# Performance work log

Hardware: AMD Instinct MI355X
Metric: run time of the kernel (lower is better)

The kernel has to match this reference:

```python
import jax, jax.numpy as jnp
import numpy as np

N_PTS = 524288
N_LEVELS = 16
F_PER = 2
T = 1 << 19            # log2_hashmap_size = 19
BASE_RES = 16
BOUND = 1.0
PLS = float(np.exp2(np.log2(2048.0 * BOUND / N_LEVELS) / (N_LEVELS - 1)))
RES = [int(np.floor(BASE_RES * PLS ** l)) for l in range(N_LEVELS)]
OFFS = np.array([[(i >> 2) & 1, (i >> 1) & 1, i & 1] for i in range(8)], dtype=np.int32)  # [8,3] cube corners


def hashgrid_encode(x, tables):
    # x: [N,3] in [0,1]; tables: [L, T, F]
    offs = jnp.asarray(OFFS)
    offs_b = offs.astype(bool)
    feats = []
    for l in range(N_LEVELS):
        res = RES[l]
        pos = x * (res - 1)
        p0 = jnp.floor(pos)
        frac = pos - p0                                     # [N,3]
        corners = jnp.clip(p0.astype(jnp.int32)[:, None, :] + offs[None], 0, res - 1)  # [N,8,3]
        w = jnp.prod(jnp.where(offs_b[None], frac[:, None, :], 1.0 - frac[:, None, :]), axis=-1)  # [N,8]
        if res ** 3 <= T:
            idx = corners[..., 0] + res * corners[..., 1] + res * res * corners[..., 2]
        else:
            c = corners.astype(jnp.uint32)
            idx = (c[..., 0] ^ (c[..., 1] * jnp.uint32(2654435761)) ^ (c[..., 2] * jnp.uint32(805459861))) & jnp.uint32(T - 1)
            idx = idx.astype(jnp.int32)
        feats.append(jnp.einsum('nkf,nk->nf', tables[l][idx], w))  # trilinear interp
    return jnp.concatenate(feats, axis=-1)  # [N, 32]


def sh_encode(d):
    # degree-4 spherical harmonics basis, torch-ngp coefficients -> [N,16]
    x, y, z = d[..., 0], d[..., 1], d[..., 2]
    xy, xz, yz = x * y, x * z, y * z
    x2, y2, z2 = x * x, y * y, z * z
    return jnp.stack([
        jnp.full_like(x, 0.28209479177387814),
        -0.48860251190291987 * y,
        0.48860251190291987 * z,
        -0.48860251190291987 * x,
        1.0925484305920792 * xy,
        -1.0925484305920792 * yz,
        0.94617469575755997 * z2 - 0.31539156525252005,
        -1.0925484305920792 * xz,
        0.54627421529603959 * (x2 - y2),
        0.59004358992664352 * y * (-3.0 * x2 + y2),
        2.8906114426405538 * xy * z,
        0.45704579946446572 * y * (1.0 - 5.0 * z2),
        0.3731763325901154 * z * (5.0 * z2 - 3.0),
        0.45704579946446572 * x * (1.0 - 5.0 * z2),
        1.4453057213202769 * z * (x2 - y2),
        0.59004358992664352 * x * (x2 - 3.0 * y2),
    ], axis=-1)


def l2_normalize(v):
    return v / jnp.maximum(jnp.linalg.norm(v, axis=-1, keepdims=True), 1e-8)


def density(xyz, tables, ws0, ws1):
    xn = jnp.clip((xyz + BOUND) / (2.0 * BOUND), 0.0, 1.0)
    h = jax.nn.relu(hashgrid_encode(xn, tables) @ ws0)  # [N,64]
    h = h @ ws1                                          # [N,16]
    return h[..., 0], h[..., 1:]                         # sigma [N], geo_feat [N,15]


def setup_inputs() -> dict:
    key = jax.random.key(0)
    ks = jax.random.split(key, 11)
    x = jax.random.uniform(ks[0], (N_PTS, 6), minval=-1.0, maxval=1.0, dtype=jnp.float32)
    tables = jax.random.uniform(ks[1], (N_LEVELS, T, F_PER), minval=-1e-4, maxval=1e-4, dtype=jnp.float32)

    def lin(k, din, dout):
        s = 1.0 / float(np.sqrt(din))
        return jax.random.uniform(k, (din, dout), minval=-s, maxval=s, dtype=jnp.float32)

    return dict(
        x=x, tables=tables,
        ws0=lin(ks[2], 32, 64), ws1=lin(ks[3], 64, 16),
        wc0=lin(ks[4], 31, 64), wc1=lin(ks[5], 64, 64), wc2=lin(ks[6], 64, 3),
        wn0=lin(ks[7], 15, 64), wn1=lin(ks[8], 64, 3),
        wm0=lin(ks[9], 15, 32), bm0=jnp.zeros((32,), jnp.float32),
        wm1=lin(ks[10], 32, 1), bm1=jnp.zeros((1,), jnp.float32),
    )


def reference(x, tables, ws0, ws1, wc0, wc1, wc2, wn0, wn1, wm0, bm0, wm1, bm1):
    xyz, d = x[:, :3], x[:, 3:]

    # sigma + analytic normal = l2_normalize(-grad_x sigma)  (compute_normal=True path)
    def f(p):
        s, g = density(p, tables, ws0, ws1)
        return s.sum(), (s, g)

    (_, (sigma, geo_feat)), grad_density = jax.value_and_grad(f, has_aux=True)(xyz)
    normal = l2_normalize(-grad_density)

    # predicted normal head (bias-free 15->64->3)
    pred_normal = l2_normalize(jax.nn.relu(geo_feat @ wn0) @ wn1)

    # color head: SH(dir) ++ geo_feat -> 31->64->64->3, sigmoid
    h = jnp.concatenate([sh_encode(d), geo_feat], axis=-1)
    rgb = jax.nn.sigmoid(jax.nn.relu(jax.nn.relu(h @ wc0) @ wc1) @ wc2)

    # mirror-mask head: 15->32 LeakyReLU ->1 sigmoid (with biases)
    m = jax.nn.leaky_relu(geo_feat @ wm0 + bm0, negative_slope=0.01)
    is_mirror = jax.nn.sigmoid(m @ wm1 + bm1)

    return sigma, geo_feat, normal, pred_normal, rgb, is_mirror
```

## Files before the change

kernel.cpp:

```cpp
#include <hip/hip_runtime.h>
#include <math.h>

#define N_POINTS 524288
#define NLV      16
#define TSZ      524288
#define TMASK    (TSZ - 1)
#define ASTART   5
#define NA       (NLV - ASTART)

static_assert(NA == 11, "NA mismatch");

struct Params { int res[NLV]; };


struct Gather {
    float2 t0, t1, t2, t3, t4, t5, t6, t7;
    float fx, fy, fz;
};
struct Enc2 { float e0, e1; };
struct EncA { float e0, e1, a0x, a0y, a0z, a1x, a1y, a1z; };
struct L3v  { float lx, ly, lz; };

template<bool HASHED>
__device__ __forceinline__ Gather lv_issue(const float2* __restrict__ lt, const int res,
                                           const float xn0, const float xn1, const float xn2)
{
#pragma clang fp contract(off)
    Gather g;
    const float rf = (float)(res - 1);
    const float px = xn0 * rf, py = xn1 * rf, pz = xn2 * rf;
    const float bx = floorf(px), by = floorf(py), bz = floorf(pz);
    g.fx = px - bx; g.fy = py - by; g.fz = pz - bz;
    const int r1 = res - 1;
    const int ix = (int)bx, iy = (int)by, iz = (int)bz;
    const int cx0 = min(max(ix, 0), r1),     cx1 = min(max(ix + 1, 0), r1);
    const int cy0 = min(max(iy, 0), r1),     cy1 = min(max(iy + 1, 0), r1);
    const int cz0 = min(max(iz, 0), r1),     cz1 = min(max(iz + 1, 0), r1);
    unsigned i000, i001, i010, i011, i100, i101, i110, i111;
    if constexpr (HASHED) {
        const unsigned hx0 = (unsigned)cx0, hx1 = (unsigned)cx1;
        const unsigned hy0 = (unsigned)cy0 * 2654435761u, hy1 = (unsigned)cy1 * 2654435761u;
        const unsigned hz0 = (unsigned)cz0 * 805459861u,  hz1 = (unsigned)cz1 * 805459861u;
        const unsigned e00 = hy0 ^ hz0, e01 = hy0 ^ hz1, e10 = hy1 ^ hz0, e11 = hy1 ^ hz1;
        i000 = (hx0 ^ e00) & TMASK; i001 = (hx0 ^ e01) & TMASK;
        i010 = (hx0 ^ e10) & TMASK; i011 = (hx0 ^ e11) & TMASK;
        i100 = (hx1 ^ e00) & TMASK; i101 = (hx1 ^ e01) & TMASK;
        i110 = (hx1 ^ e10) & TMASK; i111 = (hx1 ^ e11) & TMASK;
    } else {
        const int b00 = res * (cy0 + res * cz0), b01 = res * (cy0 + res * cz1);
        const int b10 = res * (cy1 + res * cz0), b11 = res * (cy1 + res * cz1);
        i000 = (unsigned)(cx0 + b00); i001 = (unsigned)(cx0 + b01);
        i010 = (unsigned)(cx0 + b10); i011 = (unsigned)(cx0 + b11);
        i100 = (unsigned)(cx1 + b00); i101 = (unsigned)(cx1 + b01);
        i110 = (unsigned)(cx1 + b10); i111 = (unsigned)(cx1 + b11);
    }
    g.t0 = lt[i000]; g.t1 = lt[i001]; g.t2 = lt[i010]; g.t3 = lt[i011];
    g.t4 = lt[i100]; g.t5 = lt[i101]; g.t6 = lt[i110]; g.t7 = lt[i111];
    return g;
}

__device__ __forceinline__ Enc2 lv_enc(const Gather g)
{
#pragma clang fp contract(off)
    const float gx0 = 1.0f - g.fx, gx1 = g.fx;
    const float gy0 = 1.0f - g.fy, gy1 = g.fy;
    const float gz0 = 1.0f - g.fz, gz1 = g.fz;
    const float pxy00 = gx0 * gy0, pxy01 = gx0 * gy1, pxy10 = gx1 * gy0, pxy11 = gx1 * gy1;
    const float w000 = pxy00 * gz0, w001 = pxy00 * gz1, w010 = pxy01 * gz0, w011 = pxy01 * gz1;
    const float w100 = pxy10 * gz0, w101 = pxy10 * gz1, w110 = pxy11 * gz0, w111 = pxy11 * gz1;
    float e0 = 0.0f, e1 = 0.0f;
    e0 = e0 + w000 * g.t0.x; e1 = e1 + w000 * g.t0.y;
    e0 = e0 + w001 * g.t1.x; e1 = e1 + w001 * g.t1.y;
    e0 = e0 + w010 * g.t2.x; e1 = e1 + w010 * g.t2.y;
    e0 = e0 + w011 * g.t3.x; e1 = e1 + w011 * g.t3.y;
    e0 = e0 + w100 * g.t4.x; e1 = e1 + w100 * g.t4.y;
    e0 = e0 + w101 * g.t5.x; e1 = e1 + w101 * g.t5.y;
    e0 = e0 + w110 * g.t6.x; e1 = e1 + w110 * g.t6.y;
    e0 = e0 + w111 * g.t7.x; e1 = e1 + w111 * g.t7.y;
    Enc2 r; r.e0 = e0; r.e1 = e1; return r;
}

__device__ __forceinline__ EncA lv_enc_a(const Gather g)
{
#pragma clang fp contract(off)
    const float gx0 = 1.0f - g.fx, gx1 = g.fx;
    const float gy0 = 1.0f - g.fy, gy1 = g.fy;
    const float gz0 = 1.0f - g.fz, gz1 = g.fz;
    const float pxy00 = gx0 * gy0, pxy01 = gx0 * gy1, pxy10 = gx1 * gy0, pxy11 = gx1 * gy1;
    const float w000 = pxy00 * gz0, w001 = pxy00 * gz1, w010 = pxy01 * gz0, w011 = pxy01 * gz1;
    const float w100 = pxy10 * gz0, w101 = pxy10 * gz1, w110 = pxy11 * gz0, w111 = pxy11 * gz1;
    float e0 = 0.0f, e1 = 0.0f;
    e0 = e0 + w000 * g.t0.x; e1 = e1 + w000 * g.t0.y;
    e0 = e0 + w001 * g.t1.x; e1 = e1 + w001 * g.t1.y;
    e0 = e0 + w010 * g.t2.x; e1 = e1 + w010 * g.t2.y;
    e0 = e0 + w011 * g.t3.x; e1 = e1 + w011 * g.t3.y;
    e0 = e0 + w100 * g.t4.x; e1 = e1 + w100 * g.t4.y;
    e0 = e0 + w101 * g.t5.x; e1 = e1 + w101 * g.t5.y;
    e0 = e0 + w110 * g.t6.x; e1 = e1 + w110 * g.t6.y;
    e0 = e0 + w111 * g.t7.x; e1 = e1 + w111 * g.t7.y;
    const float pyz00 = gy0 * gz0, pyz01 = gy0 * gz1, pyz10 = gy1 * gz0, pyz11 = gy1 * gz1;
    const float pxz00 = gx0 * gz0, pxz01 = gx0 * gz1, pxz10 = gx1 * gz0, pxz11 = gx1 * gz1;
    float a0x = 0.f, a0y = 0.f, a0z = 0.f, a1x = 0.f, a1y = 0.f, a1z = 0.f;
    a0x = fmaf(-pyz00, g.t0.x, a0x); a1x = fmaf(-pyz00, g.t0.y, a1x);
    a0y = fmaf(-pxz00, g.t0.x, a0y); a1y = fmaf(-pxz00, g.t0.y, a1y);
    a0z = fmaf(-pxy00, g.t0.x, a0z); a1z = fmaf(-pxy00, g.t0.y, a1z);
    a0x = fmaf(-pyz01, g.t1.x, a0x); a1x = fmaf(-pyz01, g.t1.y, a1x);
    a0y = fmaf(-pxz01, g.t1.x, a0y); a1y = fmaf(-pxz01, g.t1.y, a1y);
    a0z = fmaf( pxy00, g.t1.x, a0z); a1z = fmaf( pxy00, g.t1.y, a1z);
    a0x = fmaf(-pyz10, g.t2.x, a0x); a1x = fmaf(-pyz10, g.t2.y, a1x);
    a0y = fmaf( pxz00, g.t2.x, a0y); a1y = fmaf( pxz00, g.t2.y, a1y);
    a0z = fmaf(-pxy01, g.t2.x, a0z); a1z = fmaf(-pxy01, g.t2.y, a1z);
    a0x = fmaf(-pyz11, g.t3.x, a0x); a1x = fmaf(-pyz11, g.t3.y, a1x);
    a0y = fmaf( pxz01, g.t3.x, a0y); a1y = fmaf( pxz01, g.t3.y, a1y);
    a0z = fmaf( pxy01, g.t3.x, a0z); a1z = fmaf( pxy01, g.t3.y, a1z);
    a0x = fmaf( pyz00, g.t4.x, a0x); a1x = fmaf( pyz00, g.t4.y, a1x);
    a0y = fmaf(-pxz10, g.t4.x, a0y); a1y = fmaf(-pxz10, g.t4.y, a1y);
    a0z = fmaf(-pxy10, g.t4.x, a0z); a1z = fmaf(-pxy10, g.t4.y, a1z);
    a0x = fmaf( pyz01, g.t5.x, a0x); a1x = fmaf( pyz01, g.t5.y, a1x);
    a0y = fmaf(-pxz11, g.t5.x, a0y); a1y = fmaf(-pxz11, g.t5.y, a1y);
    a0z = fmaf( pxy10, g.t5.x, a0z); a1z = fmaf( pxy10, g.t5.y, a1z);
    a0x = fmaf( pyz10, g.t6.x, a0x); a1x = fmaf( pyz10, g.t6.y, a1x);
    a0y = fmaf( pxz10, g.t6.x, a0y); a1y = fmaf( pxz10, g.t6.y, a1y);
    a0z = fmaf(-pxy11, g.t6.x, a0z); a1z = fmaf(-pxy11, g.t6.y, a1z);
    a0x = fmaf( pyz11, g.t7.x, a0x); a1x = fmaf( pyz11, g.t7.y, a1x);
    a0y = fmaf( pxz11, g.t7.x, a0y); a1y = fmaf( pxz11, g.t7.y, a1y);
    a0z = fmaf( pxy11, g.t7.x, a0z); a1z = fmaf( pxy11, g.t7.y, a1z);
    EncA r;
    r.e0 = e0; r.e1 = e1;
    r.a0x = a0x; r.a0y = a0y; r.a0z = a0z;
    r.a1x = a1x; r.a1y = a1y; r.a1z = a1z;
    return r;
}

__device__ __forceinline__ L3v bwd_part(const Gather g, const float g0, const float g1)
{
    const float gx0 = 1.0f - g.fx, gx1 = g.fx;
    const float gy0 = 1.0f - g.fy, gy1 = g.fy;
    const float gz0 = 1.0f - g.fz, gz1 = g.fz;
    const float pyz00 = gy0 * gz0, pyz01 = gy0 * gz1, pyz10 = gy1 * gz0, pyz11 = gy1 * gz1;
    const float pxz00 = gx0 * gz0, pxz01 = gx0 * gz1, pxz10 = gx1 * gz0, pxz11 = gx1 * gz1;
    const float pxy00 = gx0 * gy0, pxy01 = gx0 * gy1, pxy10 = gx1 * gy0, pxy11 = gx1 * gy1;
    const float s000 = fmaf(g0, g.t0.x, g1 * g.t0.y);
    const float s001 = fmaf(g0, g.t1.x, g1 * g.t1.y);
    const float s010 = fmaf(g0, g.t2.x, g1 * g.t2.y);
    const float s011 = fmaf(g0, g.t3.x, g1 * g.t3.y);
    const float s100 = fmaf(g0, g.t4.x, g1 * g.t4.y);
    const float s101 = fmaf(g0, g.t5.x, g1 * g.t5.y);
    const float s110 = fmaf(g0, g.t6.x, g1 * g.t6.y);
    const float s111 = fmaf(g0, g.t7.x, g1 * g.t7.y);
    float lx = 0.f, ly = 0.f, lz = 0.f;
    lx = fmaf(-pyz00, s000, lx); ly = fmaf(-pxz00, s000, ly); lz = fmaf(-pxy00, s000, lz);
    lx = fmaf(-pyz01, s001, lx); ly = fmaf(-pxz01, s001, ly); lz = fmaf( pxy00, s001, lz);
    lx = fmaf(-pyz10, s010, lx); ly = fmaf( pxz00, s010, ly); lz = fmaf(-pxy01, s010, lz);
    lx = fmaf(-pyz11, s011, lx); ly = fmaf( pxz01, s011, ly); lz = fmaf( pxy01, s011, lz);
    lx = fmaf( pyz00, s100, lx); ly = fmaf(-pxz10, s100, ly); lz = fmaf(-pxy10, s100, lz);
    lx = fmaf( pyz01, s101, lx); ly = fmaf(-pxz11, s101, ly); lz = fmaf( pxy10, s101, lz);
    lx = fmaf( pyz10, s110, lx); ly = fmaf( pxz10, s110, ly); lz = fmaf(-pxy11, s110, lz);
    lx = fmaf( pyz11, s111, lx); ly = fmaf( pxz11, s111, ly); lz = fmaf( pxy11, s111, lz);
    L3v r; r.lx = lx; r.ly = ly; r.lz = lz; return r;
}

__device__ __forceinline__ void clampedxn(const float* __restrict__ x, const int n,
                                          float& xn0, float& xn1, float& xn2)
{
    const float x0 = x[(size_t)n * 6 + 0];
    const float x1 = x[(size_t)n * 6 + 1];
    const float x2 = x[(size_t)n * 6 + 2];
    xn0 = fminf(fmaxf((x0 + 1.0f) * 0.5f, 0.0f), 1.0f);
    xn1 = fminf(fmaxf((x1 + 1.0f) * 0.5f, 0.0f), 1.0f);
    xn2 = fminf(fmaxf((x2 + 1.0f) * 0.5f, 0.0f), 1.0f);
}

#define ST_E(L, R) { we[(size_t)(2*(L))*N + n] = R.e0; we[(size_t)(2*(L)+1)*N + n] = R.e1; }
#define ST_A(L, R) { const int i_ = (L) - ASTART;                         \
        wa[(size_t)(0*NA + i_)*N + n] = R.a0x;                            \
        wa[(size_t)(1*NA + i_)*N + n] = R.a0y;                            \
        wa[(size_t)(2*NA + i_)*N + n] = R.a0z;                            \
        wa[(size_t)(3*NA + i_)*N + n] = R.a1x;                            \
        wa[(size_t)(4*NA + i_)*N + n] = R.a1y;                            \
        wa[(size_t)(5*NA + i_)*N + n] = R.a1z; }
#define PAIR_NN(LA, LB) {                                                              \
        const Gather gA = lv_issue<false>(tb + (size_t)(LA)*TSZ, P.res[LA], xn0, xn1, xn2); \
        const Gather gB = lv_issue<false>(tb + (size_t)(LB)*TSZ, P.res[LB], xn0, xn1, xn2); \
        const Enc2 rA = lv_enc(gA); ST_E(LA, rA)                                       \
        const Enc2 rB = lv_enc(gB); ST_E(LB, rB) }
#define PAIR_NA(LA, LB) {                                                              \
        const Gather gA = lv_issue<false>(tb + (size_t)(LA)*TSZ, P.res[LA], xn0, xn1, xn2); \
        const Gather gB = lv_issue<false>(tb + (size_t)(LB)*TSZ, P.res[LB], xn0, xn1, xn2); \
        const Enc2 rA = lv_enc(gA); ST_E(LA, rA)                                       \
        const EncA rB = lv_enc_a(gB); ST_E(LB, rB) ST_A(LB, rB) }
#define PAIR_AA(LA, LB) {                                                              \
        const Gather gA = lv_issue<true>(tb + (size_t)(LA)*TSZ, P.res[LA], xn0, xn1, xn2);  \
        const Gather gB = lv_issue<true>(tb + (size_t)(LB)*TSZ, P.res[LB], xn0, xn1, xn2);  \
        const EncA rA = lv_enc_a(gA); ST_E(LA, rA) ST_A(LA, rA)                        \
        const EncA rB = lv_enc_a(gB); ST_E(LB, rB) ST_A(LB, rB) }

__global__ __launch_bounds__(256) __attribute__((amdgpu_waves_per_eu(6, 6)))
void k_gather_lo(const float* __restrict__ x, const float* __restrict__ tables,
                 float* __restrict__ ws, Params P)
{
    const int n = blockIdx.x * 256 + threadIdx.x;
    if (n >= N_POINTS) return;
    const size_t N = (size_t)N_POINTS;
    float xn0, xn1, xn2;
    clampedxn(x, n, xn0, xn1, xn2);
    const float2* __restrict__ tb = (const float2*)tables;
    float* __restrict__ we = ws;
    float* __restrict__ wa = ws + 32 * N;

    PAIR_NN(0, 1)
    PAIR_NN(2, 3)
    PAIR_NA(4, 5)
    PAIR_AA(6, 7)
}

__global__ __launch_bounds__(256) __attribute__((amdgpu_waves_per_eu(6, 6)))
void k_gather_hi(const float* __restrict__ x, const float* __restrict__ tables,
                 float* __restrict__ ws, Params P)
{
    const int n = blockIdx.x * 256 + threadIdx.x;
    if (n >= N_POINTS) return;
    const size_t N = (size_t)N_POINTS;
    float xn0, xn1, xn2;
    clampedxn(x, n, xn0, xn1, xn2);
    const float2* __restrict__ tb = (const float2*)tables;
    float* __restrict__ we = ws;
    float* __restrict__ wa = ws + 32 * N;

    PAIR_AA(8, 9)
    PAIR_AA(10, 11)
    PAIR_AA(12, 13)
    PAIR_AA(14, 15)
}

__global__ __launch_bounds__(256) __attribute__((amdgpu_waves_per_eu(5, 8)))
void k_density(const float* __restrict__ x, const float* __restrict__ tables,
               const float* __restrict__ w_s0, const float* __restrict__ w_s1,
               const float* __restrict__ ws, float* __restrict__ wgeo,
               float* __restrict__ out, Params P)
{
    const int n = blockIdx.x * 256 + threadIdx.x;
    if (n >= N_POINTS) return;
    const size_t N = (size_t)N_POINTS;
    float xn0, xn1, xn2;
    clampedxn(x, n, xn0, xn1, xn2);
    const float2* __restrict__ tb = (const float2*)tables;
    const float* __restrict__ we = ws;
    const float* __restrict__ wa = ws + 32 * N;

    float enc[32];
    #pragma unroll
    for (int j = 0; j < 32; ++j) enc[j] = we[(size_t)j * N + n];

    float hd[16];
    #pragma unroll
    for (int m = 0; m < 16; ++m) hd[m] = 0.0f;
    unsigned long long mask = 0ull;
    {
        #pragma clang fp contract(off)
        for (int k = 0; k < 64; ++k) {
            float a = 0.0f;
            #pragma unroll
            for (int j = 0; j < 32; ++j) {
                const float p = enc[j] * w_s0[j * 64 + k];
                a = a + p;
            }
            const float hr = fmaxf(a, 0.0f);
            #pragma unroll
            for (int m = 0; m < 16; ++m) hd[m] = fmaf(hr, w_s1[k * 16 + m], hd[m]);
            if (a > 0.0f) mask |= (1ull << k);
        }
    }
    const float sigma = hd[0];

    out[n] = sigma;
    #pragma unroll
    for (int j = 0; j < 15; ++j) {
        out[N + (size_t)n * 15 + j] = hd[1 + j];
        wgeo[(size_t)j * N + n] = hd[1 + j];
    }

    float genc[32];
    #pragma unroll
    for (int j = 0; j < 32; ++j) genc[j] = 0.0f;
    for (int k = 0; k < 64; ++k) {
        const float ghk = ((mask >> k) & 1ull) ? w_s1[k * 16] : 0.0f;
        #pragma unroll
        for (int j = 0; j < 32; ++j) genc[j] = fmaf(w_s0[j * 64 + k], ghk, genc[j]);
    }

    float gx = 0.0f, gy = 0.0f, gz = 0.0f;
    {
        const Gather gA = lv_issue<false>(tb + 0 * (size_t)TSZ, P.res[0], xn0, xn1, xn2);
        const Gather gB = lv_issue<false>(tb + 1 * (size_t)TSZ, P.res[1], xn0, xn1, xn2);
        {
            const L3v d = bwd_part(gA, genc[0], genc[1]);
            const float rf = (float)(P.res[0] - 1);
            gx = fmaf(d.lx, rf, gx); gy = fmaf(d.ly, rf, gy); gz = fmaf(d.lz, rf, gz);
        }
        {
            const L3v d = bwd_part(gB, genc[2], genc[3]);
            const float rf = (float)(P.res[1] - 1);
            gx = fmaf(d.lx, rf, gx); gy = fmaf(d.ly, rf, gy); gz = fmaf(d.lz, rf, gz);
        }
    }
    {
        const Gather gA = lv_issue<false>(tb + 2 * (size_t)TSZ, P.res[2], xn0, xn1, xn2);
        const Gather gB = lv_issue<false>(tb + 3 * (size_t)TSZ, P.res[3], xn0, xn1, xn2);
        {
            const L3v d = bwd_part(gA, genc[4], genc[5]);
            const float rf = (float)(P.res[2] - 1);
            gx = fmaf(d.lx, rf, gx); gy = fmaf(d.ly, rf, gy); gz = fmaf(d.lz, rf, gz);
        }
        {
            const L3v d = bwd_part(gB, genc[6], genc[7]);
            const float rf = (float)(P.res[3] - 1);
            gx = fmaf(d.lx, rf, gx); gy = fmaf(d.ly, rf, gy); gz = fmaf(d.lz, rf, gz);
        }
    }
    {
        const Gather gA = lv_issue<false>(tb + 4 * (size_t)TSZ, P.res[4], xn0, xn1, xn2);
        const L3v d = bwd_part(gA, genc[8], genc[9]);
        const float rf = (float)(P.res[4] - 1);
        gx = fmaf(d.lx, rf, gx); gy = fmaf(d.ly, rf, gy); gz = fmaf(d.lz, rf, gz);
    }

    #pragma unroll
    for (int l = ASTART; l < NLV; ++l) {
        const int i = l - ASTART;
        const float rf = (float)(P.res[l] - 1);
        const float g0 = genc[2 * l], g1 = genc[2 * l + 1];
        const float a0x = wa[(size_t)(0*NA + i)*N + n];
        const float a0y = wa[(size_t)(1*NA + i)*N + n];
        const float a0z = wa[(size_t)(2*NA + i)*N + n];
        const float a1x = wa[(size_t)(3*NA + i)*N + n];
        const float a1y = wa[(size_t)(4*NA + i)*N + n];
        const float a1z = wa[(size_t)(5*NA + i)*N + n];
        gx = fmaf(rf, fmaf(g0, a0x, g1 * a1x), gx);
        gy = fmaf(rf, fmaf(g0, a0y, g1 * a1y), gy);
        gz = fmaf(rf, fmaf(g0, a0z, g1 * a1z), gz);
    }
    gx *= 0.5f; gy *= 0.5f; gz *= 0.5f;

    const float gnorm = sqrtf(gx * gx + gy * gy + gz * gz);
    const float ginv = 1.0f / fmaxf(gnorm, 1e-8f);

    out[16 * N + (size_t)n * 3 + 0] = -gx * ginv;
    out[16 * N + (size_t)n * 3 + 1] = -gy * ginv;
    out[16 * N + (size_t)n * 3 + 2] = -gz * ginv;
}

__global__ __launch_bounds__(256) __attribute__((amdgpu_waves_per_eu(4, 4)))
void k_color(const float* __restrict__ x,
             const float* __restrict__ wc0, const float* __restrict__ wc1,
             const float* __restrict__ wc2,
             const float* __restrict__ wn0, const float* __restrict__ wn1,
             const float* __restrict__ wm0, const float* __restrict__ bm0,
             const float* __restrict__ wm1, const float* __restrict__ bm1,
             const float* __restrict__ wgeo, float* __restrict__ out)
{
    const int n = blockIdx.x * 256 + threadIdx.x;
    if (n >= N_POINTS) return;
    const size_t N = (size_t)N_POINTS;

    float geo[15];
    #pragma unroll
    for (int j = 0; j < 15; ++j) geo[j] = wgeo[(size_t)j * N + n];

    float pn0 = 0.0f, pn1 = 0.0f, pn2 = 0.0f;
    for (int k = 0; k < 64; ++k) {
        float a = 0.0f;
        #pragma unroll
        for (int j = 0; j < 15; ++j) a = fmaf(geo[j], wn0[j * 64 + k], a);
        a = fmaxf(a, 0.0f);
        pn0 = fmaf(a, wn1[k * 3 + 0], pn0);
        pn1 = fmaf(a, wn1[k * 3 + 1], pn1);
        pn2 = fmaf(a, wn1[k * 3 + 2], pn2);
    }
    const float pnorm = sqrtf(pn0 * pn0 + pn1 * pn1 + pn2 * pn2);
    const float pinv = 1.0f / fmaxf(pnorm, 1e-8f);
    out[19 * N + (size_t)n * 3 + 0] = pn0 * pinv;
    out[19 * N + (size_t)n * 3 + 1] = pn1 * pinv;
    out[19 * N + (size_t)n * 3 + 2] = pn2 * pinv;

    float macc = 0.0f;
    for (int k = 0; k < 32; ++k) {
        float a = bm0[k];
        #pragma unroll
        for (int j = 0; j < 15; ++j) a = fmaf(geo[j], wm0[j * 32 + k], a);
        a = (a >= 0.0f) ? a : 0.01f * a;
        macc = fmaf(a, wm1[k], macc);
    }
    macc += bm1[0];
    out[25 * N + n] = 1.0f / (1.0f + expf(-macc));

    const float dx = x[(size_t)n * 6 + 3];
    const float dy = x[(size_t)n * 6 + 4];
    const float dz = x[(size_t)n * 6 + 5];
    float sh[16];
    const float xy = dx * dy, xz = dx * dz, yz = dy * dz;
    const float x2s = dx * dx, y2s = dy * dy, z2s = dz * dz;
    sh[0]  = 0.28209479177387814f;
    sh[1]  = -0.48860251190291987f * dy;
    sh[2]  =  0.48860251190291987f * dz;
    sh[3]  = -0.48860251190291987f * dx;
    sh[4]  =  1.0925484305920792f * xy;
    sh[5]  = -1.0925484305920792f * yz;
    sh[6]  =  0.94617469575756f * z2s - 0.31539156525252005f;
    sh[7]  = -1.0925484305920792f * xz;
    sh[8]  =  0.5462742152960396f * (x2s - y2s);
    sh[9]  =  0.5900435899266435f * dy * (-3.0f * x2s + y2s);
    sh[10] =  2.890611442640554f * xy * dz;
    sh[11] =  0.4570457994644657f * dy * (1.0f - 5.0f * z2s);
    sh[12] =  0.3731763325901154f * dz * (5.0f * z2s - 3.0f);
    sh[13] =  0.4570457994644657f * dx * (1.0f - 5.0f * z2s);
    sh[14] =  1.445305721320277f * dz * (x2s - y2s);
    sh[15] =  0.5900435899266435f * dx * (x2s - 3.0f * y2s);

    float cacc[64];
    #pragma unroll
    for (int k = 0; k < 64; ++k) cacc[k] = 0.0f;
    for (int kc = 0; kc < 64; ++kc) {
        float a = 0.0f;
        #pragma unroll
        for (int j = 0; j < 16; ++j) a = fmaf(sh[j], wc0[j * 64 + kc], a);
        #pragma unroll
        for (int j = 0; j < 15; ++j) a = fmaf(geo[j], wc0[(16 + j) * 64 + kc], a);
        const float c1v = fmaxf(a, 0.0f);
        const float* __restrict__ wrow = wc1 + kc * 64;
        #pragma unroll
        for (int k2 = 0; k2 < 64; ++k2) cacc[k2] = fmaf(c1v, wrow[k2], cacc[k2]);
    }
    float r0 = 0.0f, r1 = 0.0f, r2 = 0.0f;
    #pragma unroll
    for (int k = 0; k < 64; ++k) {
        const float a = fmaxf(cacc[k], 0.0f);
        r0 = fmaf(a, wc2[k * 3 + 0], r0);
        r1 = fmaf(a, wc2[k * 3 + 1], r1);
        r2 = fmaf(a, wc2[k * 3 + 2], r2);
    }
    out[22 * N + (size_t)n * 3 + 0] = 1.0f / (1.0f + expf(-r0));
    out[22 * N + (size_t)n * 3 + 1] = 1.0f / (1.0f + expf(-r1));
    out[22 * N + (size_t)n * 3 + 2] = 1.0f / (1.0f + expf(-r2));
}

__global__ __launch_bounds__(256) __attribute__((amdgpu_waves_per_eu(3, 4)))
void nerf_mono(const float* __restrict__ x, const float* __restrict__ tables,
               const float* __restrict__ w_s0, const float* __restrict__ w_s1,
               const float* __restrict__ wc0, const float* __restrict__ wc1,
               const float* __restrict__ wc2, const float* __restrict__ wn0,
               const float* __restrict__ wn1, const float* __restrict__ wm0,
               const float* __restrict__ bm0, const float* __restrict__ wm1,
               const float* __restrict__ bm1, float* __restrict__ out, Params P)
{
    const int n = blockIdx.x * 256 + threadIdx.x;
    if (n >= N_POINTS) return;
    float xn0, xn1, xn2;
    clampedxn(x, n, xn0, xn1, xn2);
    const float2* __restrict__ tb = (const float2*)tables;

    float enc[32];
    float A0x[NA], A0y[NA], A0z[NA], A1x[NA], A1y[NA], A1z[NA];

#define MPAIR_NN(LA, LB) {                                                             \
        const Gather gA = lv_issue<false>(tb + (size_t)(LA)*TSZ, P.res[LA], xn0, xn1, xn2); \
        const Gather gB = lv_issue<false>(tb + (size_t)(LB)*TSZ, P.res[LB], xn0, xn1, xn2); \
        const Enc2 rA = lv_enc(gA); enc[2*(LA)] = rA.e0; enc[2*(LA)+1] = rA.e1;        \
        const Enc2 rB = lv_enc(gB); enc[2*(LB)] = rB.e0; enc[2*(LB)+1] = rB.e1; }
#define MPAIR_NA(LA, LB) {                                                             \
        const Gather gA = lv_issue<false>(tb + (size_t)(LA)*TSZ, P.res[LA], xn0, xn1, xn2); \
        const Gather gB = lv_issue<false>(tb + (size_t)(LB)*TSZ, P.res[LB], xn0, xn1, xn2); \
        const Enc2 rA = lv_enc(gA); enc[2*(LA)] = rA.e0; enc[2*(LA)+1] = rA.e1;        \
        const EncA rB = lv_enc_a(gB); enc[2*(LB)] = rB.e0; enc[2*(LB)+1] = rB.e1;      \
        A0x[(LB)-ASTART] = rB.a0x; A0y[(LB)-ASTART] = rB.a0y; A0z[(LB)-ASTART] = rB.a0z; \
        A1x[(LB)-ASTART] = rB.a1x; A1y[(LB)-ASTART] = rB.a1y; A1z[(LB)-ASTART] = rB.a1z; }
#define MPAIR_AA(LA, LB) {                                                             \
        const Gather gA = lv_issue<true>(tb + (size_t)(LA)*TSZ, P.res[LA], xn0, xn1, xn2);  \
        const Gather gB = lv_issue<true>(tb + (size_t)(LB)*TSZ, P.res[LB], xn0, xn1, xn2);  \
        const EncA rA = lv_enc_a(gA); enc[2*(LA)] = rA.e0; enc[2*(LA)+1] = rA.e1;      \
        A0x[(LA)-ASTART] = rA.a0x; A0y[(LA)-ASTART] = rA.a0y; A0z[(LA)-ASTART] = rA.a0z; \
        A1x[(LA)-ASTART] = rA.a1x; A1y[(LA)-ASTART] = rA.a1y; A1z[(LA)-ASTART] = rA.a1z; \
        const EncA rB = lv_enc_a(gB); enc[2*(LB)] = rB.e0; enc[2*(LB)+1] = rB.e1;      \
        A0x[(LB)-ASTART] = rB.a0x; A0y[(LB)-ASTART] = rB.a0y; A0z[(LB)-ASTART] = rB.a0z; \
        A1x[(LB)-ASTART] = rB.a1x; A1y[(LB)-ASTART] = rB.a1y; A1z[(LB)-ASTART] = rB.a1z; }

    MPAIR_NN(0, 1)
    MPAIR_NN(2, 3)
    MPAIR_NA(4, 5)
    MPAIR_AA(6, 7)
    MPAIR_AA(8, 9)
    MPAIR_AA(10, 11)
    MPAIR_AA(12, 13)
    MPAIR_AA(14, 15)
#undef MPAIR_NN
#undef MPAIR_NA
#undef MPAIR_AA

    float hd[16];
    #pragma unroll
    for (int m = 0; m < 16; ++m) hd[m] = 0.0f;
    unsigned long long mask = 0ull;
    {
        #pragma clang fp contract(off)
        for (int k = 0; k < 64; ++k) {
            float a = 0.0f;
            #pragma unroll
            for (int j = 0; j < 32; ++j) {
                const float p = enc[j] * w_s0[j * 64 + k];
                a = a + p;
            }
            const float hr = fmaxf(a, 0.0f);
            #pragma unroll
            for (int m = 0; m < 16; ++m) hd[m] = fmaf(hr, w_s1[k * 16 + m], hd[m]);
            if (a > 0.0f) mask |= (1ull << k);
        }
    }
    const float sigma = hd[0];

    float gx = 0.0f, gy = 0.0f, gz = 0.0f;
    {
        const Gather g0v = lv_issue<false>(tb + 0 * (size_t)TSZ, P.res[0], xn0, xn1, xn2);
        const Gather g1v = lv_issue<false>(tb + 1 * (size_t)TSZ, P.res[1], xn0, xn1, xn2);

        float genc[32];
        #pragma unroll
        for (int j = 0; j < 32; ++j) genc[j] = 0.0f;
        for (int k = 0; k < 64; ++k) {
            const float ghk = ((mask >> k) & 1ull) ? w_s1[k * 16] : 0.0f;
            #pragma unroll
            for (int j = 0; j < 32; ++j) genc[j] = fmaf(w_s0[j * 64 + k], ghk, genc[j]);
        }

        {
            const L3v d = bwd_part(g0v, genc[0], genc[1]);
            const float rf = (float)(P.res[0] - 1);
            gx = fmaf(d.lx, rf, gx); gy = fmaf(d.ly, rf, gy); gz = fmaf(d.lz, rf, gz);
        }
        {
            const L3v d = bwd_part(g1v, genc[2], genc[3]);
            const float rf = (float)(P.res[1] - 1);
            gx = fmaf(d.lx, rf, gx); gy = fmaf(d.ly, rf, gy); gz = fmaf(d.lz, rf, gz);
        }
        {
            const Gather g2v = lv_issue<false>(tb + 2 * (size_t)TSZ, P.res[2], xn0, xn1, xn2);
            const Gather g3v = lv_issue<false>(tb + 3 * (size_t)TSZ, P.res[3], xn0, xn1, xn2);
            {
                const L3v d = bwd_part(g2v, genc[4], genc[5]);
                const float rf = (float)(P.res[2] - 1);
                gx = fmaf(d.lx, rf, gx); gy = fmaf(d.ly, rf, gy); gz = fmaf(d.lz, rf, gz);
            }
            {
                const L3v d = bwd_part(g3v, genc[6], genc[7]);
                const float rf = (float)(P.res[3] - 1);
                gx = fmaf(d.lx, rf, gx); gy = fmaf(d.ly, rf, gy); gz = fmaf(d.lz, rf, gz);
            }
        }
        {
            const Gather g4v = lv_issue<false>(tb + 4 * (size_t)TSZ, P.res[4], xn0, xn1, xn2);
            const L3v d = bwd_part(g4v, genc[8], genc[9]);
            const float rf = (float)(P.res[4] - 1);
            gx = fmaf(d.lx, rf, gx); gy = fmaf(d.ly, rf, gy); gz = fmaf(d.lz, rf, gz);
        }

        #pragma unroll
        for (int l = ASTART; l < NLV; ++l) {
            const int i = l - ASTART;
            const float rf = (float)(P.res[l] - 1);
            const float g0 = genc[2 * l], g1 = genc[2 * l + 1];
            gx = fmaf(rf, fmaf(g0, A0x[i], g1 * A1x[i]), gx);
            gy = fmaf(rf, fmaf(g0, A0y[i], g1 * A1y[i]), gy);
            gz = fmaf(rf, fmaf(g0, A0z[i], g1 * A1z[i]), gz);
        }
    }
    gx *= 0.5f; gy *= 0.5f; gz *= 0.5f;

    const float gnorm = sqrtf(gx * gx + gy * gy + gz * gz);
    const float ginv = 1.0f / fmaxf(gnorm, 1e-8f);

    float geo[15];
    #pragma unroll
    for (int j = 0; j < 15; ++j) geo[j] = hd[1 + j];

    float pn0 = 0.0f, pn1 = 0.0f, pn2 = 0.0f;
    for (int k = 0; k < 64; ++k) {
        float a = 0.0f;
        #pragma unroll
        for (int j = 0; j < 15; ++j) a = fmaf(geo[j], wn0[j * 64 + k], a);
        a = fmaxf(a, 0.0f);
        pn0 = fmaf(a, wn1[k * 3 + 0], pn0);
        pn1 = fmaf(a, wn1[k * 3 + 1], pn1);
        pn2 = fmaf(a, wn1[k * 3 + 2], pn2);
    }
    const float pnorm = sqrtf(pn0 * pn0 + pn1 * pn1 + pn2 * pn2);
    const float pinv = 1.0f / fmaxf(pnorm, 1e-8f);

    const float dx = x[(size_t)n * 6 + 3];
    const float dy = x[(size_t)n * 6 + 4];
    const float dz = x[(size_t)n * 6 + 5];
    float sh[16];
    const float xy = dx * dy, xz = dx * dz, yz = dy * dz;
    const float x2s = dx * dx, y2s = dy * dy, z2s = dz * dz;
    sh[0]  = 0.28209479177387814f;
    sh[1]  = -0.48860251190291987f * dy;
    sh[2]  =  0.48860251190291987f * dz;
    sh[3]  = -0.48860251190291987f * dx;
    sh[4]  =  1.0925484305920792f * xy;
    sh[5]  = -1.0925484305920792f * yz;
    sh[6]  =  0.94617469575756f * z2s - 0.31539156525252005f;
    sh[7]  = -1.0925484305920792f * xz;
    sh[8]  =  0.5462742152960396f * (x2s - y2s);
    sh[9]  =  0.5900435899266435f * dy * (-3.0f * x2s + y2s);
    sh[10] =  2.890611442640554f * xy * dz;
    sh[11] =  0.4570457994644657f * dy * (1.0f - 5.0f * z2s);
    sh[12] =  0.3731763325901154f * dz * (5.0f * z2s - 3.0f);
    sh[13] =  0.4570457994644657f * dx * (1.0f - 5.0f * z2s);
    sh[14] =  1.445305721320277f * dz * (x2s - y2s);
    sh[15] =  0.5900435899266435f * dx * (x2s - 3.0f * y2s);

    float cacc[64];
    #pragma unroll
    for (int k = 0; k < 64; ++k) cacc[k] = 0.0f;
    for (int kc = 0; kc < 64; ++kc) {
        float a = 0.0f;
        #pragma unroll
        for (int j = 0; j < 16; ++j) a = fmaf(sh[j], wc0[j * 64 + kc], a);
        #pragma unroll
        for (int j = 0; j < 15; ++j) a = fmaf(geo[j], wc0[(16 + j) * 64 + kc], a);
        const float c1v = fmaxf(a, 0.0f);
        const float* __restrict__ wrow = wc1 + kc * 64;
        #pragma unroll
        for (int k2 = 0; k2 < 64; ++k2) cacc[k2] = fmaf(c1v, wrow[k2], cacc[k2]);
    }
    float r0 = 0.0f, r1 = 0.0f, r2 = 0.0f;
    #pragma unroll
    for (int k = 0; k < 64; ++k) {
        const float a = fmaxf(cacc[k], 0.0f);
        r0 = fmaf(a, wc2[k * 3 + 0], r0);
        r1 = fmaf(a, wc2[k * 3 + 1], r1);
        r2 = fmaf(a, wc2[k * 3 + 2], r2);
    }
    const float rgb0 = 1.0f / (1.0f + expf(-r0));
    const float rgb1 = 1.0f / (1.0f + expf(-r1));
    const float rgb2 = 1.0f / (1.0f + expf(-r2));

    float macc = 0.0f;
    for (int k = 0; k < 32; ++k) {
        float a = bm0[k];
        #pragma unroll
        for (int j = 0; j < 15; ++j) a = fmaf(geo[j], wm0[j * 32 + k], a);
        a = (a >= 0.0f) ? a : 0.01f * a;
        macc = fmaf(a, wm1[k], macc);
    }
    macc += bm1[0];
    const float mir = 1.0f / (1.0f + expf(-macc));

    const size_t N = (size_t)N_POINTS;
    out[n] = sigma;
    #pragma unroll
    for (int j = 0; j < 15; ++j)
        out[N + (size_t)n * 15 + j] = geo[j];
    out[16 * N + (size_t)n * 3 + 0] = -gx * ginv;
    out[16 * N + (size_t)n * 3 + 1] = -gy * ginv;
    out[16 * N + (size_t)n * 3 + 2] = -gz * ginv;
    out[19 * N + (size_t)n * 3 + 0] = pn0 * pinv;
    out[19 * N + (size_t)n * 3 + 1] = pn1 * pinv;
    out[19 * N + (size_t)n * 3 + 2] = pn2 * pinv;
    out[22 * N + (size_t)n * 3 + 0] = rgb0;
    out[22 * N + (size_t)n * 3 + 1] = rgb1;
    out[22 * N + (size_t)n * 3 + 2] = rgb2;
    out[25 * N + n] = mir;
}

extern "C" void kernel_launch(void* const* d_in, const int* in_sizes, int n_in,
                              void* d_out, int out_size, void* d_ws, size_t ws_size,
                              hipStream_t stream)
{
    Params P;
    const double PLS = exp2(log2(2048.0 * 1.0 / 16.0) / 15.0);
    for (int l = 0; l < NLV; ++l)
        P.res[l] = (int)floor(16.0 * pow(PLS, (double)l));

    const float* x      = (const float*)d_in[0];
    const float* tables = (const float*)d_in[1];
    const float* w_s0   = (const float*)d_in[2];
    const float* w_s1   = (const float*)d_in[3];
    const float* wc0    = (const float*)d_in[4];
    const float* wc1    = (const float*)d_in[5];
    const float* wc2    = (const float*)d_in[6];
    const float* wn0    = (const float*)d_in[7];
    const float* wn1    = (const float*)d_in[8];
    const float* wm0    = (const float*)d_in[9];
    const float* bm0    = (const float*)d_in[10];
    const float* wm1    = (const float*)d_in[11];
    const float* bm1    = (const float*)d_in[12];
    float* out = (float*)d_out;

    const size_t N = (size_t)N_POINTS;
    const size_t need = (size_t)(32 + 66 + 15) * N * sizeof(float);

    if (d_ws != nullptr && ws_size >= need) {
        float* ws   = (float*)d_ws;
        float* wgeo = ws + (size_t)98 * N;
        k_gather_lo<<<N_POINTS / 256, 256, 0, stream>>>(x, tables, ws, P);
        k_gather_hi<<<N_POINTS / 256, 256, 0, stream>>>(x, tables, ws, P);
        k_density  <<<N_POINTS / 256, 256, 0, stream>>>(x, tables, w_s0, w_s1,
                                                        ws, wgeo, out, P);
        k_color    <<<N_POINTS / 256, 256, 0, stream>>>(x, wc0, wc1, wc2,
                                                        wn0, wn1, wm0, bm0, wm1, bm1,
                                                        wgeo, out);
    } else {
        nerf_mono<<<N_POINTS / 256, 256, 0, stream>>>(x, tables, w_s0, w_s1,
                                                      wc0, wc1, wc2, wn0, wn1,
                                                      wm0, bm0, wm1, bm1, out, P);
    }
}
```

Baseline: 887.6 us.

## Replace two gather kernels with one level-major phased gather kernel

Merges the lo/hi gather kernels into a single launch where each block handles one level for 256 points, with blocks ordered level-major so that at any time the GPU mostly touches one 4 MB level table. The aim is to keep the active table resident in L2/MALL and cut cache thrashing from random gathers across many levels. In exchange, every point's coordinates are reloaded 16 times, each thread has less memory-level parallelism (8 loads instead of 16 per pair), and hashing becomes a runtime branch. It also changes occupancy hints (gather 8 waves, density fixed at 4).

```diff
diff --git a/kernel.cpp b/kernel.cpp
--- a/kernel.cpp
+++ b/kernel.cpp
@@ -21,9 +21,9 @@
 struct EncA { float e0, e1, a0x, a0y, a0z, a1x, a1y, a1z; };
 struct L3v  { float lx, ly, lz; };
 
-template<bool HASHED>
-__device__ __forceinline__ Gather lv_issue(const float2* __restrict__ lt, const int res,
-                                           const float xn0, const float xn1, const float xn2)
+__device__ __forceinline__ Gather lv_issue_rt(const float2* __restrict__ lt, const int res,
+                                              const bool hashed,
+                                              const float xn0, const float xn1, const float xn2)
 {
 #pragma clang fp contract(off)
     Gather g;
@@ -37,7 +37,7 @@
     const int cy0 = min(max(iy, 0), r1),     cy1 = min(max(iy + 1, 0), r1);
     const int cz0 = min(max(iz, 0), r1),     cz1 = min(max(iz + 1, 0), r1);
     unsigned i000, i001, i010, i011, i100, i101, i110, i111;
-    if constexpr (HASHED) {
+    if (hashed) {
         const unsigned hx0 = (unsigned)cx0, hx1 = (unsigned)cx1;
         const unsigned hy0 = (unsigned)cy0 * 2654435761u, hy1 = (unsigned)cy1 * 2654435761u;
         const unsigned hz0 = (unsigned)cz0 * 805459861u,  hz1 = (unsigned)cz1 * 805459861u;
@@ -57,6 +57,13 @@
     g.t0 = lt[i000]; g.t1 = lt[i001]; g.t2 = lt[i010]; g.t3 = lt[i011];
     g.t4 = lt[i100]; g.t5 = lt[i101]; g.t6 = lt[i110]; g.t7 = lt[i111];
     return g;
+}
+
+template<bool HASHED>
+__device__ __forceinline__ Gather lv_issue(const float2* __restrict__ lt, const int res,
+                                           const float xn0, const float xn1, const float xn2)
+{
+    return lv_issue_rt(lt, res, HASHED, xn0, xn1, xn2);
 }
 
 __device__ __forceinline__ Enc2 lv_enc(const Gather g)
@@ -171,35 +178,12 @@
     xn2 = fminf(fmaxf((x2 + 1.0f) * 0.5f, 0.0f), 1.0f);
 }
 
-#define ST_E(L, R) { we[(size_t)(2*(L))*N + n] = R.e0; we[(size_t)(2*(L)+1)*N + n] = R.e1; }
-#define ST_A(L, R) { const int i_ = (L) - ASTART;                         \
-        wa[(size_t)(0*NA + i_)*N + n] = R.a0x;                            \
-        wa[(size_t)(1*NA + i_)*N + n] = R.a0y;                            \
-        wa[(size_t)(2*NA + i_)*N + n] = R.a0z;                            \
-        wa[(size_t)(3*NA + i_)*N + n] = R.a1x;                            \
-        wa[(size_t)(4*NA + i_)*N + n] = R.a1y;                            \
-        wa[(size_t)(5*NA + i_)*N + n] = R.a1z; }
-#define PAIR_NN(LA, LB) {                                                              \
-        const Gather gA = lv_issue<false>(tb + (size_t)(LA)*TSZ, P.res[LA], xn0, xn1, xn2); \
-        const Gather gB = lv_issue<false>(tb + (size_t)(LB)*TSZ, P.res[LB], xn0, xn1, xn2); \
-        const Enc2 rA = lv_enc(gA); ST_E(LA, rA)                                       \
-        const Enc2 rB = lv_enc(gB); ST_E(LB, rB) }
-#define PAIR_NA(LA, LB) {                                                              \
-        const Gather gA = lv_issue<false>(tb + (size_t)(LA)*TSZ, P.res[LA], xn0, xn1, xn2); \
-        const Gather gB = lv_issue<false>(tb + (size_t)(LB)*TSZ, P.res[LB], xn0, xn1, xn2); \
-        const Enc2 rA = lv_enc(gA); ST_E(LA, rA)                                       \
-        const EncA rB = lv_enc_a(gB); ST_E(LB, rB) ST_A(LB, rB) }
-#define PAIR_AA(LA, LB) {                                                              \
-        const Gather gA = lv_issue<true>(tb + (size_t)(LA)*TSZ, P.res[LA], xn0, xn1, xn2);  \
-        const Gather gB = lv_issue<true>(tb + (size_t)(LB)*TSZ, P.res[LB], xn0, xn1, xn2);  \
-        const EncA rA = lv_enc_a(gA); ST_E(LA, rA) ST_A(LA, rA)                        \
-        const EncA rB = lv_enc_a(gB); ST_E(LB, rB) ST_A(LB, rB) }
-
-__global__ __launch_bounds__(256) __attribute__((amdgpu_waves_per_eu(6, 6)))
-void k_gather_lo(const float* __restrict__ x, const float* __restrict__ tables,
-                 float* __restrict__ ws, Params P)
-{
-    const int n = blockIdx.x * 256 + threadIdx.x;
+__global__ __launch_bounds__(256) __attribute__((amdgpu_waves_per_eu(8, 8)))
+void k_gather_phased(const float* __restrict__ x, const float* __restrict__ tables,
+                     float* __restrict__ ws, Params P)
+{
+    const int lvl = blockIdx.x >> 11;
+    const int n = ((blockIdx.x & 2047) << 8) + threadIdx.x;
     if (n >= N_POINTS) return;
     const size_t N = (size_t)N_POINTS;
     float xn0, xn1, xn2;
@@ -208,32 +192,29 @@
     float* __restrict__ we = ws;
     float* __restrict__ wa = ws + 32 * N;
 
-    PAIR_NN(0, 1)
-    PAIR_NN(2, 3)
-    PAIR_NA(4, 5)
-    PAIR_AA(6, 7)
-}
-
-__global__ __launch_bounds__(256) __attribute__((amdgpu_waves_per_eu(6, 6)))
-void k_gather_hi(const float* __restrict__ x, const float* __restrict__ tables,
-                 float* __restrict__ ws, Params P)
-{
-    const int n = blockIdx.x * 256 + threadIdx.x;
-    if (n >= N_POINTS) return;
-    const size_t N = (size_t)N_POINTS;
-    float xn0, xn1, xn2;
-    clampedxn(x, n, xn0, xn1, xn2);
-    const float2* __restrict__ tb = (const float2*)tables;
-    float* __restrict__ we = ws;
-    float* __restrict__ wa = ws + 32 * N;
-
-    PAIR_AA(8, 9)
-    PAIR_AA(10, 11)
-    PAIR_AA(12, 13)
-    PAIR_AA(14, 15)
-}
-
-__global__ __launch_bounds__(256) __attribute__((amdgpu_waves_per_eu(5, 8)))
+    const int res = P.res[lvl];
+    const bool hashed = (long long)res * res * res > (long long)TSZ;
+    const Gather g = lv_issue_rt(tb + (size_t)lvl * TSZ, res, hashed, xn0, xn1, xn2);
+
+    if (lvl >= ASTART) {
+        const EncA r = lv_enc_a(g);
+        we[(size_t)(2 * lvl) * N + n] = r.e0;
+        we[(size_t)(2 * lvl + 1) * N + n] = r.e1;
+        const int i_ = lvl - ASTART;
+        wa[(size_t)(0 * NA + i_) * N + n] = r.a0x;
+        wa[(size_t)(1 * NA + i_) * N + n] = r.a0y;
+        wa[(size_t)(2 * NA + i_) * N + n] = r.a0z;
+        wa[(size_t)(3 * NA + i_) * N + n] = r.a1x;
+        wa[(size_t)(4 * NA + i_) * N + n] = r.a1y;
+        wa[(size_t)(5 * NA + i_) * N + n] = r.a1z;
+    } else {
+        const Enc2 r = lv_enc(g);
+        we[(size_t)(2 * lvl) * N + n] = r.e0;
+        we[(size_t)(2 * lvl + 1) * N + n] = r.e1;
+    }
+}
+
+__global__ __launch_bounds__(256) __attribute__((amdgpu_waves_per_eu(4, 4)))
 void k_density(const float* __restrict__ x, const float* __restrict__ tables,
                const float* __restrict__ w_s0, const float* __restrict__ w_s1,
                const float* __restrict__ ws, float* __restrict__ wgeo,
@@ -701,13 +682,12 @@
     if (d_ws != nullptr && ws_size >= need) {
         float* ws   = (float*)d_ws;
         float* wgeo = ws + (size_t)98 * N;
-        k_gather_lo<<<N_POINTS / 256, 256, 0, stream>>>(x, tables, ws, P);
-        k_gather_hi<<<N_POINTS / 256, 256, 0, stream>>>(x, tables, ws, P);
-        k_density  <<<N_POINTS / 256, 256, 0, stream>>>(x, tables, w_s0, w_s1,
-                                                        ws, wgeo, out, P);
-        k_color    <<<N_POINTS / 256, 256, 0, stream>>>(x, wc0, wc1, wc2,
-                                                        wn0, wn1, wm0, bm0, wm1, bm1,
-                                                        wgeo, out);
+        k_gather_phased<<<NLV * (N_POINTS / 256), 256, 0, stream>>>(x, tables, ws, P);
+        k_density<<<N_POINTS / 256, 256, 0, stream>>>(x, tables, w_s0, w_s1,
+                                                      ws, wgeo, out, P);
+        k_color  <<<N_POINTS / 256, 256, 0, stream>>>(x, wc0, wc1, wc2,
+                                                      wn0, wn1, wm0, bm0, wm1, bm1,
+                                                      wgeo, out);
     } else {
         nerf_mono<<<N_POINTS / 256, 256, 0, stream>>>(x, tables, w_s0, w_s1,
                                                       wc0, wc1, wc2, wn0, wn1,
```

Result: faster. 770.4 us (-13.2%).
